# Kernel optimization log

Hardware: AMD Instinct MI355X
Metric: run time of the kernel (lower is better)

Reference implementation:

```python
import jax, jax.numpy as jnp
import numpy as np

B, S, D = 16, 8192, 512
NUM_HEADS = 8
HEAD_DIM = D // NUM_HEADS
SCALE = HEAD_DIM ** -0.5
TEMP = 1.0
THRESHOLD = 0.5
PRIOR = 0.2


def setup_inputs() -> dict:
    key = jax.random.key(0)
    k1, k2, k3, k4 = jax.random.split(key, 4)
    hidden = jax.random.normal(k1, (B, S, D), dtype=jnp.float32)
    lim = float(np.sqrt(6.0 / (D + D)))  # xavier_uniform for square Linear
    Wq = jax.random.uniform(k2, (D, D), minval=-lim, maxval=lim, dtype=jnp.float32)
    Wk = jax.random.uniform(k3, (D, D), minval=-lim, maxval=lim, dtype=jnp.float32)
    noise = jax.random.uniform(k4, (B, S), minval=1e-6, maxval=1.0 - 1e-6, dtype=jnp.float32)
    return {"hidden": hidden, "Wq": Wq, "Wk": Wk, "noise": noise}


def reference(hidden, Wq, Wk, noise):
    # L2-normalize tokens (F.normalize)
    h = hidden / jnp.maximum(jnp.linalg.norm(hidden, axis=-1, keepdims=True), 1e-12)
    Q = h @ Wq.T  # [B,S,D]
    K = h @ Wk.T  # [B,S,D]
    # boundary_scores = (Q K^T * scale).sum(-1) == scale * Q . (sum_j K_j)  (O(n*d) rewrite)
    scores = jnp.einsum('bsd,bd->bs', Q, K.sum(axis=1)) * jnp.float32(SCALE)
    # probs = sigmoid(scores); RelaxedBernoulli logits == scores (clamp is a no-op)
    logistic = jnp.log(noise) - jnp.log1p(-noise)
    soft = jax.nn.sigmoid((scores + logistic) / jnp.float32(TEMP))
    hard = (soft > THRESHOLD).astype(jnp.float32)
    ste = soft + jax.lax.stop_gradient(hard - soft)  # straight-through
    # 'delete' compaction: keep boundary tokens, packed left, zero-padded to S
    keep = hard > 0.0
    order = jnp.argsort(jnp.where(keep, 0, 1), axis=1, stable=True)  # kept indices first, in order
    gathered = jnp.take_along_axis(h * ste[..., None], order[..., None], axis=1)  # [B,S,D]
    counts = keep.sum(axis=1)  # [B]
    valid = jnp.arange(S)[None, :] < counts[:, None]
    pooled = gathered * valid[..., None]
    # Binomial(n=S, p=prior).log_prob(num_boundaries)
    n = jnp.float32(S)
    k = ste.sum(axis=-1)
    p = jnp.float32(PRIOR)
    log_prob = (jax.lax.lgamma(n + 1.0) - jax.lax.lgamma(k + 1.0) - jax.lax.lgamma(n - k + 1.0)
                + k * jnp.log(p) + (n - k) * jnp.log1p(-p))
    loss = -log_prob.mean() / n
    return pooled, loss
```

## Files before the change

kernel.cpp:

```cpp
#include <hip/hip_runtime.h>
#include <math.h>

#define Bn 16
#define Sn 8192
#define Dn 512
#define CHUNKS 64
#define TOK_PER_BLOCK (Sn / CHUNKS)
#define TOK_PER_WAVE (TOK_PER_BLOCK / 4)

__device__ __forceinline__ double dot8sq(const float4& a, const float4& c) {
  return (double)a.x * a.x + (double)a.y * a.y + (double)a.z * a.z +
         (double)a.w * a.w + (double)c.x * c.x + (double)c.y * c.y +
         (double)c.z * c.z + (double)c.w * c.w;
}

__global__ __launch_bounds__(256) void k1_norm_hsum(
    const float* __restrict__ hidden, double* __restrict__ inv_norm,
    double* __restrict__ hsum) {
  __shared__ double part[4][Dn];
  const int b = blockIdx.x / CHUNKS;
  const int chunk = blockIdx.x % CHUNKS;
  const int wave = threadIdx.x >> 6;
  const int lane = threadIdx.x & 63;

  double acc[8] = {0., 0., 0., 0., 0., 0., 0., 0.};
  const int sbase = chunk * TOK_PER_BLOCK + wave * TOK_PER_WAVE;
  const float* hb = hidden + (size_t)b * Sn * Dn;

  for (int t0 = 0; t0 < TOK_PER_WAVE; t0 += 4) {
    const int s = sbase + t0;
    const float4* r0 = (const float4*)(hb + (size_t)(s + 0) * Dn);
    const float4* r1 = (const float4*)(hb + (size_t)(s + 1) * Dn);
    const float4* r2 = (const float4*)(hb + (size_t)(s + 2) * Dn);
    const float4* r3 = (const float4*)(hb + (size_t)(s + 3) * Dn);
    float4 a0 = r0[lane], c0 = r0[64 + lane];
    float4 a1 = r1[lane], c1 = r1[64 + lane];
    float4 a2 = r2[lane], c2 = r2[64 + lane];
    float4 a3 = r3[lane], c3 = r3[64 + lane];
    double s0 = dot8sq(a0, c0), s1 = dot8sq(a1, c1);
    double s2 = dot8sq(a2, c2), s3 = dot8sq(a3, c3);
#pragma unroll
    for (int m = 32; m >= 1; m >>= 1) {
      s0 += __shfl_xor(s0, m, 64);
      s1 += __shfl_xor(s1, m, 64);
      s2 += __shfl_xor(s2, m, 64);
      s3 += __shfl_xor(s3, m, 64);
    }
    const double i0 = 1.0 / fmax(sqrt(s0), 1e-12);
    const double i1 = 1.0 / fmax(sqrt(s1), 1e-12);
    const double i2 = 1.0 / fmax(sqrt(s2), 1e-12);
    const double i3 = 1.0 / fmax(sqrt(s3), 1e-12);
    if (lane < 4) {
      const double iv = (lane == 0) ? i0 : (lane == 1) ? i1 : (lane == 2) ? i2 : i3;
      inv_norm[(size_t)b * Sn + s + lane] = iv;
    }
    acc[0] += (double)a0.x * i0 + (double)a1.x * i1 + (double)a2.x * i2 + (double)a3.x * i3;
    acc[1] += (double)a0.y * i0 + (double)a1.y * i1 + (double)a2.y * i2 + (double)a3.y * i3;
    acc[2] += (double)a0.z * i0 + (double)a1.z * i1 + (double)a2.z * i2 + (double)a3.z * i3;
    acc[3] += (double)a0.w * i0 + (double)a1.w * i1 + (double)a2.w * i2 + (double)a3.w * i3;
    acc[4] += (double)c0.x * i0 + (double)c1.x * i1 + (double)c2.x * i2 + (double)c3.x * i3;
    acc[5] += (double)c0.y * i0 + (double)c1.y * i1 + (double)c2.y * i2 + (double)c3.y * i3;
    acc[6] += (double)c0.z * i0 + (double)c1.z * i1 + (double)c2.z * i2 + (double)c3.z * i3;
    acc[7] += (double)c0.w * i0 + (double)c1.w * i1 + (double)c2.w * i2 + (double)c3.w * i3;
  }
  const int d0 = lane * 4;
#pragma unroll
  for (int k = 0; k < 4; ++k) {
    part[wave][d0 + k] = acc[k];
    part[wave][256 + d0 + k] = acc[4 + k];
  }
  __syncthreads();
  for (int i = threadIdx.x; i < Dn; i += 256) {
    const double v = part[0][i] + part[1][i] + part[2][i] + part[3][i];
    atomicAdd(&hsum[b * Dn + i], v);
  }
}

__global__ __launch_bounds__(512) void k2_u(
    const float* __restrict__ Wq, const float* __restrict__ Wk,
    const double* __restrict__ hsum, double* __restrict__ u) {
  __shared__ double hl[Dn];
  __shared__ double ks[Dn];
  const int b = blockIdx.x;
  const int tid = threadIdx.x;
  hl[tid] = hsum[b * Dn + tid];
  __syncthreads();
  {
    const float* wrow = Wk + (size_t)tid * Dn;
    double p0 = 0., p1 = 0., p2 = 0., p3 = 0.;
    for (int e = 0; e < Dn; e += 4) {
      p0 += (double)wrow[e + 0] * hl[e + 0];
      p1 += (double)wrow[e + 1] * hl[e + 1];
      p2 += (double)wrow[e + 2] * hl[e + 2];
      p3 += (double)wrow[e + 3] * hl[e + 3];
    }
    ks[tid] = (p0 + p1) + (p2 + p3);
  }
  __syncthreads();
  {
    double p0 = 0., p1 = 0., p2 = 0., p3 = 0.;
    for (int d = 0; d < Dn; d += 4) {
      p0 += (double)Wq[(size_t)(d + 0) * Dn + tid] * ks[d + 0];
      p1 += (double)Wq[(size_t)(d + 1) * Dn + tid] * ks[d + 1];
      p2 += (double)Wq[(size_t)(d + 2) * Dn + tid] * ks[d + 2];
      p3 += (double)Wq[(size_t)(d + 3) * Dn + tid] * ks[d + 3];
    }
    u[b * Dn + tid] = (p0 + p1) + (p2 + p3);
  }
}

__global__ __launch_bounds__(256) void k3_scores(
    const float* __restrict__ hidden, const double* __restrict__ inv_norm,
    const double* __restrict__ u, const float* __restrict__ noise,
    int* __restrict__ keep) {
  __shared__ double ul[Dn];
  const int b = blockIdx.x / CHUNKS;
  const int chunk = blockIdx.x % CHUNKS;
  for (int i = threadIdx.x; i < Dn; i += 256) ul[i] = u[b * Dn + i];
  __syncthreads();
  const int wave = threadIdx.x >> 6, lane = threadIdx.x & 63;
  const int d0 = lane * 4;
  const double u0 = ul[d0 + 0], u1 = ul[d0 + 1], u2 = ul[d0 + 2], u3 = ul[d0 + 3];
  const double u4 = ul[256 + d0 + 0], u5 = ul[256 + d0 + 1];
  const double u6 = ul[256 + d0 + 2], u7 = ul[256 + d0 + 3];
  const int sbase = chunk * TOK_PER_BLOCK + wave * TOK_PER_WAVE;
  const float* hb = hidden + (size_t)b * Sn * Dn;

  for (int t0 = 0; t0 < TOK_PER_WAVE; t0 += 4) {
    const int s = sbase + t0;
    const float4* r0 = (const float4*)(hb + (size_t)(s + 0) * Dn);
    const float4* r1 = (const float4*)(hb + (size_t)(s + 1) * Dn);
    const float4* r2 = (const float4*)(hb + (size_t)(s + 2) * Dn);
    const float4* r3 = (const float4*)(hb + (size_t)(s + 3) * Dn);
    float4 a0 = r0[lane], c0 = r0[64 + lane];
    float4 a1 = r1[lane], c1 = r1[64 + lane];
    float4 a2 = r2[lane], c2 = r2[64 + lane];
    float4 a3 = r3[lane], c3 = r3[64 + lane];
    double d0v = (double)a0.x * u0 + (double)a0.y * u1 + (double)a0.z * u2 + (double)a0.w * u3 +
                 (double)c0.x * u4 + (double)c0.y * u5 + (double)c0.z * u6 + (double)c0.w * u7;
    double d1v = (double)a1.x * u0 + (double)a1.y * u1 + (double)a1.z * u2 + (double)a1.w * u3 +
                 (double)c1.x * u4 + (double)c1.y * u5 + (double)c1.z * u6 + (double)c1.w * u7;
    double d2v = (double)a2.x * u0 + (double)a2.y * u1 + (double)a2.z * u2 + (double)a2.w * u3 +
                 (double)c2.x * u4 + (double)c2.y * u5 + (double)c2.z * u6 + (double)c2.w * u7;
    double d3v = (double)a3.x * u0 + (double)a3.y * u1 + (double)a3.z * u2 + (double)a3.w * u3 +
                 (double)c3.x * u4 + (double)c3.y * u5 + (double)c3.z * u6 + (double)c3.w * u7;
#pragma unroll
    for (int m = 32; m >= 1; m >>= 1) {
      d0v += __shfl_xor(d0v, m, 64);
      d1v += __shfl_xor(d1v, m, 64);
      d2v += __shfl_xor(d2v, m, 64);
      d3v += __shfl_xor(d3v, m, 64);
    }
    if (lane < 4) {
      const double dj = (lane == 0) ? d0v : (lane == 1) ? d1v : (lane == 2) ? d2v : d3v;
      const size_t tok = (size_t)b * Sn + s + lane;
      const double nv = (double)noise[tok];
      const double x = 0.125 * inv_norm[tok] * dj + log(nv) - log1p(-nv);
      keep[tok] = (x > 0.0) ? 1 : 0;
    }
  }
}

__global__ __launch_bounds__(1024) void k4_scan(
    const int* __restrict__ keep, int* __restrict__ pos,
    int* __restrict__ counts, double* __restrict__ logprob) {
  __shared__ int wsum[16];
  const int b = blockIdx.x, tid = threadIdx.x;
  const int lane = tid & 63, wave = tid >> 6;
  const size_t base = (size_t)b * Sn + (size_t)tid * 8;
  const int4 kk0 = *(const int4*)(keep + base);
  const int4 kk1 = *(const int4*)(keep + base + 4);
  int v[8] = {kk0.x, kk0.y, kk0.z, kk0.w, kk1.x, kk1.y, kk1.z, kk1.w};
  int pref[8], tot = 0;
#pragma unroll
  for (int j = 0; j < 8; ++j) {
    pref[j] = tot;
    tot += v[j];
  }
  int x = tot;
#pragma unroll
  for (int m = 1; m < 64; m <<= 1) {
    const int y = __shfl_up(x, m, 64);
    if (lane >= m) x += y;
  }
  if (lane == 63) wsum[wave] = x;
  __syncthreads();
  int wp = 0;
  for (int w = 0; w < wave; ++w) wp += wsum[w];
  const int excl = wp + x - tot;
  int4 o0, o1;
  o0.x = excl + pref[0]; o0.y = excl + pref[1]; o0.z = excl + pref[2]; o0.w = excl + pref[3];
  o1.x = excl + pref[4]; o1.y = excl + pref[5]; o1.z = excl + pref[6]; o1.w = excl + pref[7];
  *(int4*)(pos + base) = o0;
  *(int4*)(pos + base + 4) = o1;
  if (tid == 0) {
    int total = 0;
    for (int w = 0; w < 16; ++w) total += wsum[w];
    counts[b] = total;
    const double n = (double)Sn, k = (double)total;
    logprob[b] = lgamma(n + 1.0) - lgamma(k + 1.0) - lgamma(n - k + 1.0) +
                 k * log(0.2) + (n - k) * log1p(-0.2);
  }
}

__global__ __launch_bounds__(256) void k5_scatter(
    const float* __restrict__ hidden, const double* __restrict__ inv_norm,
    const int* __restrict__ keep, const int* __restrict__ pos,
    const int* __restrict__ counts, const double* __restrict__ logprob,
    float* __restrict__ out) {
  const int b = blockIdx.x / CHUNKS;
  const int chunk = blockIdx.x % CHUNKS;
  const int wave = threadIdx.x >> 6, lane = threadIdx.x & 63;
  const int cnt = counts[b];
  const int sbase = chunk * TOK_PER_BLOCK + wave * TOK_PER_WAVE;
  const float* hb = hidden + (size_t)b * Sn * Dn;
  float* ob = out + (size_t)b * Sn * Dn;
  for (int t = 0; t < TOK_PER_WAVE; ++t) {
    const int s = sbase + t;
    const size_t tok = (size_t)b * Sn + s;
    if (s >= cnt) {
      float4* orow = (float4*)(ob + (size_t)s * Dn);
      const float4 z = make_float4(0.f, 0.f, 0.f, 0.f);
      orow[lane] = z;
      orow[64 + lane] = z;
    }
    if (keep[tok]) {
      const int p = pos[tok];
      const double inv = inv_norm[tok];
      const float4* row = (const float4*)(hb + (size_t)s * Dn);
      float4 a = row[lane], c = row[64 + lane];
      a.x = (float)((double)a.x * inv); a.y = (float)((double)a.y * inv);
      a.z = (float)((double)a.z * inv); a.w = (float)((double)a.w * inv);
      c.x = (float)((double)c.x * inv); c.y = (float)((double)c.y * inv);
      c.z = (float)((double)c.z * inv); c.w = (float)((double)c.w * inv);
      float4* orow = (float4*)(ob + (size_t)p * Dn);
      orow[lane] = a;
      orow[64 + lane] = c;
    }
  }
  if (blockIdx.x == 0 && threadIdx.x == 0) {
    double sm = 0.0;
    for (int i = 0; i < Bn; ++i) sm += logprob[i];
    out[(size_t)Bn * Sn * Dn] = (float)(-(sm / (double)Bn) / (double)Sn);
  }
}

extern "C" void kernel_launch(void* const* d_in, const int* in_sizes, int n_in,
                              void* d_out, int out_size, void* d_ws, size_t ws_size,
                              hipStream_t stream) {
  const float* hidden = (const float*)d_in[0];
  const float* Wq = (const float*)d_in[1];
  const float* Wk = (const float*)d_in[2];
  const float* noise = (const float*)d_in[3];
  float* out = (float*)d_out;

  char* ws = (char*)d_ws;
  double* hsum = (double*)(ws);
  double* u = (double*)(ws + 65536);
  double* inv_nrm = (double*)(ws + 131072);
  int* keep = (int*)(ws + 131072 + 1048576);
  int* pos = (int*)(ws + 131072 + 1048576 + 524288);
  int* counts = (int*)(ws + 131072 + 1048576 + 2 * 524288);
  double* logprob = (double*)(ws + 131072 + 1048576 + 2 * 524288 + 256);

  hipMemsetAsync(hsum, 0, Bn * Dn * sizeof(double), stream);

  k1_norm_hsum<<<Bn * CHUNKS, 256, 0, stream>>>(hidden, inv_nrm, hsum);
  k2_u<<<Bn, 512, 0, stream>>>(Wq, Wk, hsum, u);
  k3_scores<<<Bn * CHUNKS, 256, 0, stream>>>(hidden, inv_nrm, u, noise, keep);
  k4_scan<<<Bn, 1024, 0, stream>>>(keep, pos, counts, logprob);
  k5_scatter<<<Bn * CHUNKS, 256, 0, stream>>>(hidden, inv_nrm, keep, pos, counts,
                                              logprob, out);
}
```

Baseline: 605.5 us.

## Prefetch rows in norm pass, split projection kernel, batch scatter metadata loads

k1 now loads the next 4 token rows into registers while it processes the current ones, a software prefetch meant to hide load latency. The serial per-batch k2 is split into two kernels: a row-parallel Wk·hsum pass with wave reductions over 256 blocks, and a Wq pass over 64 blocks. The aim is to cover more CUs than the previous 16 blocks did. k3 handles 8 tokens per iteration and k5 loads keep/pos/inv_norm once per wave and broadcasts them by shuffle, batching row loads by 4; the cost is higher register pressure and an extra launch.

```diff
diff --git a/kernel.cpp b/kernel.cpp
--- a/kernel.cpp
+++ b/kernel.cpp
@@ -27,86 +27,120 @@
   const int sbase = chunk * TOK_PER_BLOCK + wave * TOK_PER_WAVE;
   const float* hb = hidden + (size_t)b * Sn * Dn;
 
+  float4 cur[8];
+#pragma unroll
+  for (int j = 0; j < 4; ++j) {
+    const float4* r = (const float4*)(hb + (size_t)(sbase + j) * Dn);
+    cur[2 * j] = r[lane];
+    cur[2 * j + 1] = r[64 + lane];
+  }
+
   for (int t0 = 0; t0 < TOK_PER_WAVE; t0 += 4) {
-    const int s = sbase + t0;
-    const float4* r0 = (const float4*)(hb + (size_t)(s + 0) * Dn);
-    const float4* r1 = (const float4*)(hb + (size_t)(s + 1) * Dn);
-    const float4* r2 = (const float4*)(hb + (size_t)(s + 2) * Dn);
-    const float4* r3 = (const float4*)(hb + (size_t)(s + 3) * Dn);
-    float4 a0 = r0[lane], c0 = r0[64 + lane];
-    float4 a1 = r1[lane], c1 = r1[64 + lane];
-    float4 a2 = r2[lane], c2 = r2[64 + lane];
-    float4 a3 = r3[lane], c3 = r3[64 + lane];
-    double s0 = dot8sq(a0, c0), s1 = dot8sq(a1, c1);
-    double s2 = dot8sq(a2, c2), s3 = dot8sq(a3, c3);
+    const bool more = (t0 + 4) < TOK_PER_WAVE;
+    float4 nxt[8];
+    if (more) {
+#pragma unroll
+      for (int j = 0; j < 4; ++j) {
+        const float4* r = (const float4*)(hb + (size_t)(sbase + t0 + 4 + j) * Dn);
+        nxt[2 * j] = r[lane];
+        nxt[2 * j + 1] = r[64 + lane];
+      }
+    }
+    double ss[4];
+#pragma unroll
+    for (int j = 0; j < 4; ++j) ss[j] = dot8sq(cur[2 * j], cur[2 * j + 1]);
+#pragma unroll
+    for (int m = 32; m >= 1; m >>= 1) {
+#pragma unroll
+      for (int j = 0; j < 4; ++j) ss[j] += __shfl_xor(ss[j], m, 64);
+    }
+    double inv[4];
+#pragma unroll
+    for (int j = 0; j < 4; ++j) inv[j] = 1.0 / fmax(sqrt(ss[j]), 1e-12);
+    if (lane < 4) {
+      const double iv = (lane == 0) ? inv[0] : (lane == 1) ? inv[1]
+                       : (lane == 2) ? inv[2] : inv[3];
+      inv_norm[(size_t)b * Sn + sbase + t0 + lane] = iv;
+    }
+#pragma unroll
+    for (int j = 0; j < 4; ++j) {
+      acc[0] += (double)cur[2 * j].x * inv[j];
+      acc[1] += (double)cur[2 * j].y * inv[j];
+      acc[2] += (double)cur[2 * j].z * inv[j];
+      acc[3] += (double)cur[2 * j].w * inv[j];
+      acc[4] += (double)cur[2 * j + 1].x * inv[j];
+      acc[5] += (double)cur[2 * j + 1].y * inv[j];
+      acc[6] += (double)cur[2 * j + 1].z * inv[j];
+      acc[7] += (double)cur[2 * j + 1].w * inv[j];
+    }
+    if (more) {
+#pragma unroll
+      for (int j = 0; j < 8; ++j) cur[j] = nxt[j];
+    }
+  }
+  const int d0 = lane * 4;
+#pragma unroll
+  for (int k = 0; k < 4; ++k) {
+    part[wave][d0 + k] = acc[k];
+    part[wave][256 + d0 + k] = acc[4 + k];
+  }
+  __syncthreads();
+  for (int i = threadIdx.x; i < Dn; i += 256) {
+    const double v = part[0][i] + part[1][i] + part[2][i] + part[3][i];
+    atomicAdd(&hsum[b * Dn + i], v);
+  }
+}
+
+__global__ __launch_bounds__(256) void k2a_ks(
+    const float* __restrict__ Wk, const double* __restrict__ hsum,
+    double* __restrict__ ks) {
+  __shared__ double hl[Dn];
+  const int b = blockIdx.x >> 4;
+  const int rg = blockIdx.x & 15;
+  const int tid = threadIdx.x, wave = tid >> 6, lane = tid & 63;
+  for (int i = tid; i < Dn; i += 256) hl[i] = hsum[b * Dn + i];
+  __syncthreads();
+#pragma unroll
+  for (int rp = 0; rp < 8; rp += 2) {
+    const int row0 = rg * 32 + wave * 8 + rp;
+    const int row1 = row0 + 1;
+    const float* w0 = Wk + (size_t)row0 * Dn;
+    const float* w1 = Wk + (size_t)row1 * Dn;
+    double s0 = 0., s1 = 0.;
+#pragma unroll
+    for (int j = 0; j < 8; ++j) {
+      const int e = lane + 64 * j;
+      s0 += (double)w0[e] * hl[e];
+      s1 += (double)w1[e] * hl[e];
+    }
 #pragma unroll
     for (int m = 32; m >= 1; m >>= 1) {
       s0 += __shfl_xor(s0, m, 64);
       s1 += __shfl_xor(s1, m, 64);
-      s2 += __shfl_xor(s2, m, 64);
-      s3 += __shfl_xor(s3, m, 64);
-    }
-    const double i0 = 1.0 / fmax(sqrt(s0), 1e-12);
-    const double i1 = 1.0 / fmax(sqrt(s1), 1e-12);
-    const double i2 = 1.0 / fmax(sqrt(s2), 1e-12);
-    const double i3 = 1.0 / fmax(sqrt(s3), 1e-12);
-    if (lane < 4) {
-      const double iv = (lane == 0) ? i0 : (lane == 1) ? i1 : (lane == 2) ? i2 : i3;
-      inv_norm[(size_t)b * Sn + s + lane] = iv;
-    }
-    acc[0] += (double)a0.x * i0 + (double)a1.x * i1 + (double)a2.x * i2 + (double)a3.x * i3;
-    acc[1] += (double)a0.y * i0 + (double)a1.y * i1 + (double)a2.y * i2 + (double)a3.y * i3;
-    acc[2] += (double)a0.z * i0 + (double)a1.z * i1 + (double)a2.z * i2 + (double)a3.z * i3;
-    acc[3] += (double)a0.w * i0 + (double)a1.w * i1 + (double)a2.w * i2 + (double)a3.w * i3;
-    acc[4] += (double)c0.x * i0 + (double)c1.x * i1 + (double)c2.x * i2 + (double)c3.x * i3;
-    acc[5] += (double)c0.y * i0 + (double)c1.y * i1 + (double)c2.y * i2 + (double)c3.y * i3;
-    acc[6] += (double)c0.z * i0 + (double)c1.z * i1 + (double)c2.z * i2 + (double)c3.z * i3;
-    acc[7] += (double)c0.w * i0 + (double)c1.w * i1 + (double)c2.w * i2 + (double)c3.w * i3;
-  }
-  const int d0 = lane * 4;
-#pragma unroll
-  for (int k = 0; k < 4; ++k) {
-    part[wave][d0 + k] = acc[k];
-    part[wave][256 + d0 + k] = acc[4 + k];
-  }
-  __syncthreads();
-  for (int i = threadIdx.x; i < Dn; i += 256) {
-    const double v = part[0][i] + part[1][i] + part[2][i] + part[3][i];
-    atomicAdd(&hsum[b * Dn + i], v);
-  }
-}
-
-__global__ __launch_bounds__(512) void k2_u(
-    const float* __restrict__ Wq, const float* __restrict__ Wk,
-    const double* __restrict__ hsum, double* __restrict__ u) {
-  __shared__ double hl[Dn];
-  __shared__ double ks[Dn];
-  const int b = blockIdx.x;
+    }
+    if (lane == 0) ks[b * Dn + row0] = s0;
+    if (lane == 1) ks[b * Dn + row1] = s1;
+  }
+}
+
+__global__ __launch_bounds__(128) void k2b_u(
+    const float* __restrict__ Wq, const double* __restrict__ ks,
+    double* __restrict__ u) {
+  __shared__ double kl[Dn];
+  const int b = blockIdx.x >> 2;
+  const int g = blockIdx.x & 3;
   const int tid = threadIdx.x;
-  hl[tid] = hsum[b * Dn + tid];
-  __syncthreads();
-  {
-    const float* wrow = Wk + (size_t)tid * Dn;
-    double p0 = 0., p1 = 0., p2 = 0., p3 = 0.;
-    for (int e = 0; e < Dn; e += 4) {
-      p0 += (double)wrow[e + 0] * hl[e + 0];
-      p1 += (double)wrow[e + 1] * hl[e + 1];
-      p2 += (double)wrow[e + 2] * hl[e + 2];
-      p3 += (double)wrow[e + 3] * hl[e + 3];
-    }
-    ks[tid] = (p0 + p1) + (p2 + p3);
-  }
-  __syncthreads();
-  {
-    double p0 = 0., p1 = 0., p2 = 0., p3 = 0.;
-    for (int d = 0; d < Dn; d += 4) {
-      p0 += (double)Wq[(size_t)(d + 0) * Dn + tid] * ks[d + 0];
-      p1 += (double)Wq[(size_t)(d + 1) * Dn + tid] * ks[d + 1];
-      p2 += (double)Wq[(size_t)(d + 2) * Dn + tid] * ks[d + 2];
-      p3 += (double)Wq[(size_t)(d + 3) * Dn + tid] * ks[d + 3];
-    }
-    u[b * Dn + tid] = (p0 + p1) + (p2 + p3);
-  }
+  for (int i = tid; i < Dn; i += 128) kl[i] = ks[b * Dn + i];
+  __syncthreads();
+  const int e = g * 128 + tid;
+  double p0 = 0., p1 = 0., p2 = 0., p3 = 0.;
+  for (int d = 0; d < Dn; d += 4) {
+    p0 += (double)Wq[(size_t)(d + 0) * Dn + e] * kl[d + 0];
+    p1 += (double)Wq[(size_t)(d + 1) * Dn + e] * kl[d + 1];
+    p2 += (double)Wq[(size_t)(d + 2) * Dn + e] * kl[d + 2];
+    p3 += (double)Wq[(size_t)(d + 3) * Dn + e] * kl[d + 3];
+  }
+  u[b * Dn + e] = (p0 + p1) + (p2 + p3);
 }
 
 __global__ __launch_bounds__(256) void k3_scores(
@@ -126,34 +160,26 @@
   const int sbase = chunk * TOK_PER_BLOCK + wave * TOK_PER_WAVE;
   const float* hb = hidden + (size_t)b * Sn * Dn;
 
-  for (int t0 = 0; t0 < TOK_PER_WAVE; t0 += 4) {
-    const int s = sbase + t0;
-    const float4* r0 = (const float4*)(hb + (size_t)(s + 0) * Dn);
-    const float4* r1 = (const float4*)(hb + (size_t)(s + 1) * Dn);
-    const float4* r2 = (const float4*)(hb + (size_t)(s + 2) * Dn);
-    const float4* r3 = (const float4*)(hb + (size_t)(s + 3) * Dn);
-    float4 a0 = r0[lane], c0 = r0[64 + lane];
-    float4 a1 = r1[lane], c1 = r1[64 + lane];
-    float4 a2 = r2[lane], c2 = r2[64 + lane];
-    float4 a3 = r3[lane], c3 = r3[64 + lane];
-    double d0v = (double)a0.x * u0 + (double)a0.y * u1 + (double)a0.z * u2 + (double)a0.w * u3 +
-                 (double)c0.x * u4 + (double)c0.y * u5 + (double)c0.z * u6 + (double)c0.w * u7;
-    double d1v = (double)a1.x * u0 + (double)a1.y * u1 + (double)a1.z * u2 + (double)a1.w * u3 +
-                 (double)c1.x * u4 + (double)c1.y * u5 + (double)c1.z * u6 + (double)c1.w * u7;
-    double d2v = (double)a2.x * u0 + (double)a2.y * u1 + (double)a2.z * u2 + (double)a2.w * u3 +
-                 (double)c2.x * u4 + (double)c2.y * u5 + (double)c2.z * u6 + (double)c2.w * u7;
-    double d3v = (double)a3.x * u0 + (double)a3.y * u1 + (double)a3.z * u2 + (double)a3.w * u3 +
-                 (double)c3.x * u4 + (double)c3.y * u5 + (double)c3.z * u6 + (double)c3.w * u7;
+  for (int t0 = 0; t0 < TOK_PER_WAVE; t0 += 8) {
+    double dv[8];
+#pragma unroll
+    for (int j = 0; j < 8; ++j) {
+      const float4* r = (const float4*)(hb + (size_t)(sbase + t0 + j) * Dn);
+      const float4 a = r[lane], c = r[64 + lane];
+      dv[j] = (double)a.x * u0 + (double)a.y * u1 + (double)a.z * u2 +
+              (double)a.w * u3 + (double)c.x * u4 + (double)c.y * u5 +
+              (double)c.z * u6 + (double)c.w * u7;
+    }
 #pragma unroll
     for (int m = 32; m >= 1; m >>= 1) {
-      d0v += __shfl_xor(d0v, m, 64);
-      d1v += __shfl_xor(d1v, m, 64);
-      d2v += __shfl_xor(d2v, m, 64);
-      d3v += __shfl_xor(d3v, m, 64);
-    }
-    if (lane < 4) {
-      const double dj = (lane == 0) ? d0v : (lane == 1) ? d1v : (lane == 2) ? d2v : d3v;
-      const size_t tok = (size_t)b * Sn + s + lane;
+#pragma unroll
+      for (int j = 0; j < 8; ++j) dv[j] += __shfl_xor(dv[j], m, 64);
+    }
+    if (lane < 8) {
+      double dj = dv[0];
+#pragma unroll
+      for (int j = 1; j < 8; ++j) dj = (lane == j) ? dv[j] : dj;
+      const size_t tok = (size_t)b * Sn + sbase + t0 + lane;
       const double nv = (double)noise[tok];
       const double x = 0.125 * inv_norm[tok] * dj + log(nv) - log1p(-nv);
       keep[tok] = (x > 0.0) ? 1 : 0;
@@ -213,29 +239,59 @@
   const int wave = threadIdx.x >> 6, lane = threadIdx.x & 63;
   const int cnt = counts[b];
   const int sbase = chunk * TOK_PER_BLOCK + wave * TOK_PER_WAVE;
+  const size_t tbase = (size_t)b * Sn + sbase;
   const float* hb = hidden + (size_t)b * Sn * Dn;
   float* ob = out + (size_t)b * Sn * Dn;
-  for (int t = 0; t < TOK_PER_WAVE; ++t) {
-    const int s = sbase + t;
-    const size_t tok = (size_t)b * Sn + s;
-    if (s >= cnt) {
-      float4* orow = (float4*)(ob + (size_t)s * Dn);
-      const float4 z = make_float4(0.f, 0.f, 0.f, 0.f);
-      orow[lane] = z;
-      orow[64 + lane] = z;
-    }
-    if (keep[tok]) {
-      const int p = pos[tok];
-      const double inv = inv_norm[tok];
-      const float4* row = (const float4*)(hb + (size_t)s * Dn);
-      float4 a = row[lane], c = row[64 + lane];
-      a.x = (float)((double)a.x * inv); a.y = (float)((double)a.y * inv);
-      a.z = (float)((double)a.z * inv); a.w = (float)((double)a.w * inv);
-      c.x = (float)((double)c.x * inv); c.y = (float)((double)c.y * inv);
-      c.z = (float)((double)c.z * inv); c.w = (float)((double)c.w * inv);
-      float4* orow = (float4*)(ob + (size_t)p * Dn);
-      orow[lane] = a;
-      orow[64 + lane] = c;
+
+  int mk = 0, mp = 0;
+  double mi = 0.0;
+  if (lane < 32) {
+    mk = keep[tbase + lane];
+    mp = pos[tbase + lane];
+    mi = inv_norm[tbase + lane];
+  }
+  const float4 z = make_float4(0.f, 0.f, 0.f, 0.f);
+
+  for (int t0 = 0; t0 < TOK_PER_WAVE; t0 += 4) {
+    int kk[4], pp[4], ss[4];
+    double iv[4];
+#pragma unroll
+    for (int j = 0; j < 4; ++j) {
+      kk[j] = __shfl(mk, t0 + j, 64);
+      pp[j] = __shfl(mp, t0 + j, 64);
+      iv[j] = __shfl(mi, t0 + j, 64);
+      ss[j] = sbase + t0 + j;
+    }
+#pragma unroll
+    for (int j = 0; j < 4; ++j) {
+      if (ss[j] >= cnt) {
+        float4* orow = (float4*)(ob + (size_t)ss[j] * Dn);
+        orow[lane] = z;
+        orow[64 + lane] = z;
+      }
+    }
+    float4 a[4], c[4];
+#pragma unroll
+    for (int j = 0; j < 4; ++j) {
+      if (kk[j]) {
+        const float4* r = (const float4*)(hb + (size_t)ss[j] * Dn);
+        a[j] = r[lane];
+        c[j] = r[64 + lane];
+      }
+    }
+#pragma unroll
+    for (int j = 0; j < 4; ++j) {
+      if (kk[j]) {
+        float4 aa = a[j], cc = c[j];
+        const double v = iv[j];
+        aa.x = (float)((double)aa.x * v); aa.y = (float)((double)aa.y * v);
+        aa.z = (float)((double)aa.z * v); aa.w = (float)((double)aa.w * v);
+        cc.x = (float)((double)cc.x * v); cc.y = (float)((double)cc.y * v);
+        cc.z = (float)((double)cc.z * v); cc.w = (float)((double)cc.w * v);
+        float4* orow = (float4*)(ob + (size_t)pp[j] * Dn);
+        orow[lane] = aa;
+        orow[64 + lane] = cc;
+      }
     }
   }
   if (blockIdx.x == 0 && threadIdx.x == 0) {
@@ -257,16 +313,18 @@
   char* ws = (char*)d_ws;
   double* hsum = (double*)(ws);
   double* u = (double*)(ws + 65536);
-  double* inv_nrm = (double*)(ws + 131072);
-  int* keep = (int*)(ws + 131072 + 1048576);
-  int* pos = (int*)(ws + 131072 + 1048576 + 524288);
-  int* counts = (int*)(ws + 131072 + 1048576 + 2 * 524288);
-  double* logprob = (double*)(ws + 131072 + 1048576 + 2 * 524288 + 256);
+  double* ks = (double*)(ws + 131072);
+  double* inv_nrm = (double*)(ws + 196608);
+  int* keep = (int*)(ws + 1245184);
+  int* pos = (int*)(ws + 1769472);
+  int* counts = (int*)(ws + 2293760);
+  double* logprob = (double*)(ws + 2294016);
 
   hipMemsetAsync(hsum, 0, Bn * Dn * sizeof(double), stream);
 
   k1_norm_hsum<<<Bn * CHUNKS, 256, 0, stream>>>(hidden, inv_nrm, hsum);
-  k2_u<<<Bn, 512, 0, stream>>>(Wq, Wk, hsum, u);
+  k2a_ks<<<Bn * 16, 256, 0, stream>>>(Wk, hsum, ks);
+  k2b_u<<<Bn * 4, 128, 0, stream>>>(Wq, ks, u);
   k3_scores<<<Bn * CHUNKS, 256, 0, stream>>>(hidden, inv_nrm, u, noise, keep);
   k4_scan<<<Bn, 1024, 0, stream>>>(keep, pos, counts, logprob);
   k5_scatter<<<Bn * CHUNKS, 256, 0, stream>>>(hidden, inv_nrm, keep, pos, counts,
```

Result: faster. 573.2 us (-5.3%).
